# Kernel tuning notes

Hardware: AMD Instinct MI355X
Metric: run time of the kernel (lower is better)

Reference implementation:

```python
import jax, jax.numpy as jnp
import numpy as np

B, C, H, W = 16, 512, 25, 25
HEADS = 8
HID = 2048
PATCH = 5  # hardcoded patch_size in FusionAttention
EPS_LN = 1e-5
EPS_BN = 1e-5


def _channel_layernorm(x, g, b):
    # torch: std = var(unbiased=False).sqrt(); (x-mean)/(std+eps)*g + b, over channel dim=1
    mean = jnp.mean(x, axis=1, keepdims=True)
    var = jnp.var(x, axis=1, keepdims=True)
    return (x - mean) / (jnp.sqrt(var) + EPS_LN) * g + b


def _dwconv3x3(x, w, b):
    # depthwise 3x3, padding 1; w: (C,1,3,3)
    y = jax.lax.conv_general_dilated(
        x, w, window_strides=(1, 1), padding=((1, 1), (1, 1)),
        feature_group_count=x.shape[1],
        dimension_numbers=('NCHW', 'OIHW', 'NCHW'))
    return y + b[None, :, None, None]


def setup_inputs() -> dict:
    key = jax.random.key(0)
    ks = jax.random.split(key, 20)
    s = 0.02
    d = {
        'x': jax.random.normal(ks[0], (B, C, H, W), jnp.float32),
        'ln1_g': jnp.ones((1, C, 1, 1), jnp.float32),
        'ln1_b': jnp.zeros((1, C, 1, 1), jnp.float32),
        'wq': jax.random.normal(ks[1], (C, 1, 3, 3), jnp.float32) * s,
        'bq': jnp.zeros((C,), jnp.float32),
        'wk': jax.random.normal(ks[2], (C, 1, 3, 3), jnp.float32) * s,
        'bk': jnp.zeros((C,), jnp.float32),
        'wv': jax.random.normal(ks[3], (C, 1, 3, 3), jnp.float32) * s,
        'bv': jnp.zeros((C,), jnp.float32),
        'swq': jax.random.normal(ks[4], (C, 1, 3, 3), jnp.float32) * s,
        'sbq': jnp.zeros((C,), jnp.float32),
        'swk': jax.random.normal(ks[5], (C, 1, 3, 3), jnp.float32) * s,
        'sbk': jnp.zeros((C,), jnp.float32),
        'swv': jax.random.normal(ks[6], (C, 1, 3, 3), jnp.float32) * s,
        'sbv': jnp.zeros((C,), jnp.float32),
        'proj_w': jax.random.normal(ks[7], (C, C, 1, 1), jnp.float32) * s,
        'bn_g': jnp.ones((C,), jnp.float32),
        'bn_b': jnp.zeros((C,), jnp.float32),
        'bn_mean': jnp.zeros((C,), jnp.float32),
        'bn_var': jnp.ones((C,), jnp.float32),
        'ln2_g': jnp.ones((1, C, 1, 1), jnp.float32),
        'ln2_b': jnp.zeros((1, C, 1, 1), jnp.float32),
        'w1': jax.random.normal(ks[8], (HID, C, 1, 1), jnp.float32) * s,
        'b1': jnp.zeros((HID,), jnp.float32),
        'w2': jax.random.normal(ks[9], (C, HID, 1, 1), jnp.float32) * s,
        'b2': jnp.zeros((C,), jnp.float32),
    }
    return d


def _fusion_attention(x, wq, bq, wk, bk, wv, bv, swq, sbq, swk, sbk, swv, sbv,
                      proj_w, bn_g, bn_b, bn_mean, bn_var):
    b, c, h, w = x.shape
    n = h * w
    hd = c // HEADS
    scale = hd ** -0.5

    def split_heads(t):  # (b,c,h,w) -> (b, heads, n, hd)
        return t.reshape(b, HEADS, hd, n).transpose(0, 1, 3, 2)

    q = split_heads(_dwconv3x3(x, wq, bq))
    k = split_heads(_dwconv3x3(x, wk, bk))
    v = split_heads(_dwconv3x3(x, wv, bv))

    dots = jnp.einsum('bhid,bhjd->bhij', q, k) * scale
    attn = jax.nn.softmax(dots, axis=-1)
    out = jnp.einsum('bhij,bhjd->bhid', attn, v)
    # rearrange 'b h (H W) d -> b (h d) H W' with H=PATCH
    out = out.transpose(0, 1, 3, 2).reshape(b, c, PATCH, n // PATCH)

    spe_q = _dwconv3x3(out, swq, sbq).reshape(b, c, n)          # b d (l w)
    spe_k = _dwconv3x3(out, swk, sbk).reshape(b, c, n).transpose(0, 2, 1)  # b (l w) d
    spe_v = _dwconv3x3(out, swv, sbv).reshape(b, c, n)

    attention = jax.nn.softmax(jnp.einsum('bcn,bnd->bcd', spe_q, spe_k) * scale, axis=-1)
    x_out = jnp.einsum('bcd,bdn->bcn', attention, spe_v).reshape(b, c, h, w)

    # 1x1 conv (no bias) + BatchNorm2d (eval mode)
    proj = jnp.einsum('oc,bchw->bohw', proj_w[:, :, 0, 0], x_out)
    proj = (proj - bn_mean[None, :, None, None]) / jnp.sqrt(bn_var + EPS_BN)[None, :, None, None]
    proj = proj * bn_g[None, :, None, None] + bn_b[None, :, None, None]
    return proj


def _feedforward(x, w1, b1, w2, b2):
    h1 = jnp.einsum('oc,bchw->bohw', w1[:, :, 0, 0], x) + b1[None, :, None, None]
    h1 = jax.nn.gelu(h1, approximate=False)
    return jnp.einsum('oc,bchw->bohw', w2[:, :, 0, 0], h1) + b2[None, :, None, None]


def reference(x, ln1_g, ln1_b, wq, bq, wk, bk, wv, bv, swq, sbq, swk, sbk,
              swv, sbv, proj_w, bn_g, bn_b, bn_mean, bn_var, ln2_g, ln2_b,
              w1, b1, w2, b2):
    y1 = x + _fusion_attention(_channel_layernorm(x, ln1_g, ln1_b),
                               wq, bq, wk, bk, wv, bv, swq, sbq, swk, sbk,
                               swv, sbv, proj_w, bn_g, bn_b, bn_mean, bn_var)
    y_out = y1 + _feedforward(_channel_layernorm(y1, ln2_g, ln2_b), w1, b1, w2, b2)
    return y_out
```

## Files before the change

### kernel.cpp

```cpp
#include <hip/hip_runtime.h>
#include <math.h>

constexpr int BATCH = 16;
constexpr int CH    = 512;
constexpr int NPIX  = 625;
constexpr int HEADS = 8;
constexpr int HDIM  = 64;
constexpr int HIDD  = 2048;

constexpr float EPS_LN = 1e-5f;
constexpr float EPS_BN = 1e-5f;
constexpr float SCALE  = 0.125f;

typedef __bf16 bf16x8 __attribute__((ext_vector_type(8)));
typedef float  f32x4  __attribute__((ext_vector_type(4)));

static __device__ inline unsigned pack_bf16(float lo, float hi) {
  union { __bf16 h; unsigned short u; } a, b;
  a.h = (__bf16)lo; b.h = (__bf16)hi;
  return ((unsigned)b.u << 16) | (unsigned)a.u;
}

__global__ __launch_bounds__(256) void ln_kernel2(
    const float* __restrict__ x, const float* __restrict__ g,
    const float* __restrict__ bt, float* __restrict__ y) {
  __shared__ float ps[4][64];
  __shared__ float pss[4][64];
  int lane = threadIdx.x & 63;
  int w    = threadIdx.x >> 6;
  int b    = blockIdx.y;
  int i    = blockIdx.x * 64 + lane;
  int ic   = i < NPIX ? i : NPIX - 1;
  const float* xb = x + (size_t)b * CH * NPIX + ic;
  float s = 0.f, ss = 0.f;
  #pragma unroll 4
  for (int c = w * 128; c < w * 128 + 128; ++c) {
    float v = xb[(size_t)c * NPIX];
    s += v; ss += v * v;
  }
  ps[w][lane] = s; pss[w][lane] = ss;
  __syncthreads();
  float st  = ps[0][lane] + ps[1][lane] + ps[2][lane] + ps[3][lane];
  float sst = pss[0][lane] + pss[1][lane] + pss[2][lane] + pss[3][lane];
  float mean = st * (1.0f / CH);
  float var  = sst * (1.0f / CH) - mean * mean;
  float inv  = 1.0f / (sqrtf(fmaxf(var, 0.0f)) + EPS_LN);
  if (i >= NPIX) return;
  float* yb = y + (size_t)b * CH * NPIX + i;
  #pragma unroll 4
  for (int c = w * 128; c < w * 128 + 128; ++c) {
    float v = xb[(size_t)c * NPIX];
    yb[(size_t)c * NPIX] = (v - mean) * inv * g[c] + bt[c];
  }
}

__global__ void dwconv3_kernel(const float* __restrict__ src,
    const float* __restrict__ w0, const float* __restrict__ b0,
    const float* __restrict__ w1, const float* __restrict__ b1,
    const float* __restrict__ w2, const float* __restrict__ b2,
    float* __restrict__ d0, float* __restrict__ d1, float* __restrict__ d2,
    int Hc, int Wc) {
  size_t idx = (size_t)blockIdx.x * blockDim.x + threadIdx.x;
  size_t total = (size_t)BATCH * CH * Hc * Wc;
  if (idx >= total) return;
  int wp = (int)(idx % Wc);
  int hp = (int)((idx / Wc) % Hc);
  int c  = (int)((idx / ((size_t)Wc * Hc)) % CH);
  const float* f0 = w0 + c * 9;
  const float* f1 = w1 + c * 9;
  const float* f2 = w2 + c * 9;
  float a0 = 0.f, a1 = 0.f, a2 = 0.f;
  #pragma unroll
  for (int kh = -1; kh <= 1; ++kh) {
    int h2 = hp + kh; if (h2 < 0 || h2 >= Hc) continue;
    #pragma unroll
    for (int kw = -1; kw <= 1; ++kw) {
      int w2p = wp + kw; if (w2p < 0 || w2p >= Wc) continue;
      float v = src[idx + (size_t)kh * Wc + kw];
      int wi = (kh + 1) * 3 + (kw + 1);
      a0 += v * f0[wi]; a1 += v * f1[wi]; a2 += v * f2[wi];
    }
  }
  d0[idx] = a0 + b0[c];
  d1[idx] = a1 + b1[c];
  d2[idx] = a2 + b2[c];
}

__global__ void dwconv_spe_kernel(const float* __restrict__ src,
    const float* __restrict__ w0, const float* __restrict__ b0,
    const float* __restrict__ w1, const float* __restrict__ b1,
    const float* __restrict__ w2, const float* __restrict__ b2,
    __bf16* __restrict__ q16, __bf16* __restrict__ k16, float* __restrict__ v) {
  size_t idx = (size_t)blockIdx.x * blockDim.x + threadIdx.x;
  if (idx >= (size_t)BATCH * CH * 640) return;
  int n = (int)(idx % 640);
  int c = (int)((idx / 640) % CH);
  int b = (int)(idx / ((size_t)640 * CH));
  if (n >= NPIX) { q16[idx] = (__bf16)0.f; k16[idx] = (__bf16)0.f; return; }
  int hp = n / 125, wp = n % 125;
  size_t base = ((size_t)b * CH + c) * NPIX;
  const float* f0 = w0 + c * 9;
  const float* f1 = w1 + c * 9;
  const float* f2 = w2 + c * 9;
  float a0 = 0.f, a1 = 0.f, a2 = 0.f;
  #pragma unroll
  for (int kh = -1; kh <= 1; ++kh) {
    int h2 = hp + kh; if (h2 < 0 || h2 >= 5) continue;
    #pragma unroll
    for (int kw = -1; kw <= 1; ++kw) {
      int w2p = wp + kw; if (w2p < 0 || w2p >= 125) continue;
      float vv = src[base + h2 * 125 + w2p];
      int wi = (kh + 1) * 3 + (kw + 1);
      a0 += vv * f0[wi]; a1 += vv * f1[wi]; a2 += vv * f2[wi];
    }
  }
  q16[idx] = (__bf16)(a0 + b0[c]);
  k16[idx] = (__bf16)(a1 + b1[c]);
  v[base + n] = a2 + b2[c];
}

__global__ __launch_bounds__(256) void qk_to_bf16T(
    const float* __restrict__ q, const float* __restrict__ k,
    __bf16* __restrict__ qT, __bf16* __restrict__ kT) {
  __shared__ __bf16 tq[64][65];
  __shared__ __bf16 tk[64][65];
  int bh = blockIdx.y;
  int n0 = blockIdx.x * 64;
  int b = bh >> 3, h = bh & 7;
  const float* qb = q + (size_t)(b * CH + h * HDIM) * NPIX;
  const float* kb = k + (size_t)(b * CH + h * HDIM) * NPIX;
  #pragma unroll
  for (int it = 0; it < 16; ++it) {
    int idx = threadIdx.x + it * 256;
    int d = idx >> 6, n = idx & 63;
    int nn = n0 + n;
    float qv = (nn < NPIX) ? qb[(size_t)d * NPIX + nn] : 0.f;
    float kv = (nn < NPIX) ? kb[(size_t)d * NPIX + nn] : 0.f;
    tq[n][d] = (__bf16)qv;
    tk[n][d] = (__bf16)kv;
  }
  __syncthreads();
  size_t obase = (size_t)bh * NPIX;
  #pragma unroll
  for (int it = 0; it < 16; ++it) {
    int idx = threadIdx.x + it * 256;
    int n = idx >> 6, d = idx & 63;
    int nn = n0 + n;
    if (nn < NPIX) {
      qT[(obase + nn) * 64 + d] = tq[n][d];
      kT[(obase + nn) * 64 + d] = tk[n][d];
    }
  }
}

__global__ void v_to_bf16(const float* __restrict__ v, __bf16* __restrict__ v16) {
  int row = blockIdx.x;
  const float* src = v + (size_t)row * NPIX;
  __bf16* dst = v16 + (size_t)row * 640;
  for (int n = threadIdx.x; n < NPIX; n += 256) dst[n] = (__bf16)src[n];
}

__global__ __launch_bounds__(64) void head_attn_mfma2(
    const __bf16* __restrict__ qT, const __bf16* __restrict__ kT,
    const __bf16* __restrict__ vB, float* __restrict__ out) {
  __shared__ __align__(16) union SmT {
    unsigned char p[16 * 1280];
    float ostage[64][17];
  } sm;
  int lane = threadIdx.x & 63;
  int g = lane >> 4, li = lane & 15;
  int h = blockIdx.y, b = blockIdx.z;
  int bh = b * HEADS + h;
  int i0 = blockIdx.x * 16;
  const __bf16* Qb = qT + (size_t)bh * NPIX * 64;
  const __bf16* Kb = kT + (size_t)bh * NPIX * 64;
  const __bf16* Vb = vB + (size_t)(b * CH + h * HDIM) * 640;

  bf16x8 aq0, aq1;
  {
    int qr = i0 + li; if (qr > NPIX - 1) qr = NPIX - 1;
    const __bf16* qp = Qb + (size_t)qr * 64 + 8 * g;
    aq0 = *(const bf16x8*)(qp);
    aq1 = *(const bf16x8*)(qp + 32);
  }

  f32x4 s[40];
  #pragma unroll
  for (int cf = 0; cf < 40; ++cf) {
    int kc = cf * 16 + li;
    int kcl = kc > NPIX - 1 ? NPIX - 1 : kc;
    const __bf16* kp = Kb + (size_t)kcl * 64 + 8 * g;
    bf16x8 bk0 = *(const bf16x8*)(kp);
    bf16x8 bk1 = *(const bf16x8*)(kp + 32);
    f32x4 acc = (f32x4){0.f, 0.f, 0.f, 0.f};
    acc = __builtin_amdgcn_mfma_f32_16x16x32_bf16(aq0, bk0, acc, 0, 0, 0);
    acc = __builtin_amdgcn_mfma_f32_16x16x32_bf16(aq1, bk1, acc, 0, 0, 0);
    s[cf] = acc * SCALE;
  }
  if (li > 0) {
    s[39][0] = -1e30f; s[39][1] = -1e30f; s[39][2] = -1e30f; s[39][3] = -1e30f;
  }

  #pragma unroll
  for (int r = 0; r < 4; ++r) {
    float mx = -1e30f;
    #pragma unroll
    for (int cf = 0; cf < 40; ++cf) mx = fmaxf(mx, s[cf][r]);
    mx = fmaxf(mx, __shfl_xor(mx, 1));
    mx = fmaxf(mx, __shfl_xor(mx, 2));
    mx = fmaxf(mx, __shfl_xor(mx, 4));
    mx = fmaxf(mx, __shfl_xor(mx, 8));
    float sum = 0.f;
    #pragma unroll
    for (int cf = 0; cf < 40; ++cf) {
      float p = __expf(s[cf][r] - mx);
      s[cf][r] = p;
      sum += p;
    }
    sum += __shfl_xor(sum, 1);
    sum += __shfl_xor(sum, 2);
    sum += __shfl_xor(sum, 4);
    sum += __shfl_xor(sum, 8);
    float inv = 1.0f / sum;
    #pragma unroll
    for (int cf = 0; cf < 40; ++cf) s[cf][r] *= inv;
  }

  #pragma unroll
  for (int cfp = 0; cfp < 20; ++cfp) {
    int cf0 = 2 * cfp, cf1 = cf0 + 1;
    #pragma unroll
    for (int r = 0; r < 4; ++r) {
      float v0 = s[cf0][r], v1 = s[cf1][r];
      float t0 = __shfl_xor(v0, 1);
      float t1 = __shfl_xor(v1, 1);
      bool even = (li & 1) == 0;
      float lo = even ? v0 : t1;
      float hi = even ? t0 : v1;
      int col_w = even ? (cf0 * 16 + li) : (cf1 * 16 + li - 1);
      int row = 4 * g + r;
      int off = (row * 1280 + col_w * 2) ^ ((row & 7) << 4);
      *(unsigned*)(&sm.p[off]) = pack_bf16(lo, hi);
    }
  }

  f32x4 o[4];
  #pragma unroll
  for (int dg = 0; dg < 4; ++dg) o[dg] = (f32x4){0.f, 0.f, 0.f, 0.f};
  #pragma unroll
  for (int ks = 0; ks < 20; ++ks) {
    int offr = (li * 1280 + ks * 64 + 16 * g) ^ ((li & 7) << 4);
    bf16x8 pa = *(const bf16x8*)(&sm.p[offr]);
    const __bf16* vp = Vb + (size_t)li * 640 + ks * 32 + 8 * g;
    #pragma unroll
    for (int dg = 0; dg < 4; ++dg) {
      bf16x8 bv = *(const bf16x8*)(vp + (size_t)dg * 16 * 640);
      o[dg] = __builtin_amdgcn_mfma_f32_16x16x32_bf16(pa, bv, o[dg], 0, 0, 0);
    }
  }

  __syncthreads();
  #pragma unroll
  for (int dg = 0; dg < 4; ++dg) {
    #pragma unroll
    for (int r = 0; r < 4; ++r)
      sm.ostage[dg * 16 + li][4 * g + r] = o[dg][r];
  }
  __syncthreads();
  size_t cbase = (size_t)(b * CH + h * HDIM);
  int n = i0 + li;
  if (n < NPIX) {
    #pragma unroll
    for (int dd = 0; dd < 16; ++dd) {
      int d = dd * 4 + g;
      out[(cbase + d) * NPIX + n] = sm.ostage[d][li];
    }
  }
}

__global__ __launch_bounds__(64) void chan_attn_mfma(
    const __bf16* __restrict__ sq, const __bf16* __restrict__ sk,
    __bf16* __restrict__ Am) {
  int lane = threadIdx.x & 63;
  int g = lane >> 4, li = lane & 15;
  int b = blockIdx.y;
  int cq0 = blockIdx.x * 16;
  const __bf16* qrow  = sq + ((size_t)b * CH + cq0 + li) * 640 + 8 * g;
  const __bf16* kbase = sk + ((size_t)b * CH + li) * 640 + 8 * g;
  f32x4 acc[32];
  #pragma unroll
  for (int i = 0; i < 32; ++i) acc[i] = (f32x4){0.f, 0.f, 0.f, 0.f};
  for (int ks = 0; ks < 20; ++ks) {
    bf16x8 af = *(const bf16x8*)(qrow + ks * 32);
    #pragma unroll
    for (int cf = 0; cf < 32; ++cf) {
      bf16x8 bfr = *(const bf16x8*)(kbase + (size_t)cf * 16 * 640 + ks * 32);
      acc[cf] = __builtin_amdgcn_mfma_f32_16x16x32_bf16(af, bfr, acc[cf], 0, 0, 0);
    }
  }
  #pragma unroll
  for (int i = 0; i < 32; ++i) acc[i] = acc[i] * SCALE;
  __bf16* Ab = Am + ((size_t)b * CH + cq0) * CH;
  #pragma unroll
  for (int r = 0; r < 4; ++r) {
    float mx = -1e30f;
    #pragma unroll
    for (int cf = 0; cf < 32; ++cf) mx = fmaxf(mx, acc[cf][r]);
    mx = fmaxf(mx, __shfl_xor(mx, 1));
    mx = fmaxf(mx, __shfl_xor(mx, 2));
    mx = fmaxf(mx, __shfl_xor(mx, 4));
    mx = fmaxf(mx, __shfl_xor(mx, 8));
    float sum = 0.f;
    #pragma unroll
    for (int cf = 0; cf < 32; ++cf) {
      float p = __expf(acc[cf][r] - mx);
      acc[cf][r] = p;
      sum += p;
    }
    sum += __shfl_xor(sum, 1);
    sum += __shfl_xor(sum, 2);
    sum += __shfl_xor(sum, 4);
    sum += __shfl_xor(sum, 8);
    float inv = 1.0f / sum;
    #pragma unroll
    for (int cf = 0; cf < 32; ++cf)
      Ab[(size_t)(4 * g + r) * CH + cf * 16 + li] = (__bf16)(acc[cf][r] * inv);
  }
}

template <int EPI>
__global__ __launch_bounds__(256) void gemm_nt(
    const __bf16* __restrict__ A, long long aBatch,
    const __bf16* __restrict__ B, long long bBatch,
    void* __restrict__ Cout, long long cBatch,
    int M, int N, int K,
    const float* __restrict__ p0, const float* __restrict__ p1,
    const float* __restrict__ res, long long resBatch) {
  __shared__ __align__(16) union {
    struct { unsigned char As[128 * 128]; unsigned char Bs[64 * 128]; } s;
    float Ce[4][64][17];
  } u;
  int t = threadIdx.x;
  int w = t >> 6, lane = t & 63, g = lane >> 4, li = lane & 15;
  int wm = w & 1, wn = w >> 1;
  int n0 = blockIdx.x * 64, m0 = blockIdx.y * 128, b = blockIdx.z;
  const __bf16* Ab = A + (size_t)b * aBatch;
  const __bf16* Bb = B + (size_t)b * bBatch;
  f32x4 acc[4][2];
  #pragma unroll
  for (int i = 0; i < 4; ++i)
    #pragma unroll
    for (int j = 0; j < 2; ++j) acc[i][j] = (f32x4){0.f, 0.f, 0.f, 0.f};

  for (int k0 = 0; k0 < K; k0 += 64) {
    bf16x8 ra[4], rb[2];
    #pragma unroll
    for (int i = 0; i < 4; ++i) {
      int e = t + i * 256;
      int row = e >> 3, cc = e & 7;
      int ar = m0 + row; ar = ar < M ? ar : M - 1;
      ra[i] = *(const bf16x8*)(Ab + (size_t)ar * K + k0 + cc * 8);
    }
    #pragma unroll
    for (int i = 0; i < 2; ++i) {
      int e = t + i * 256;
      int row = e >> 3, cc = e & 7;
      rb[i] = *(const bf16x8*)(Bb + (size_t)(n0 + row) * K + k0 + cc * 8);
    }
    __syncthreads();
    #pragma unroll
    for (int i = 0; i < 4; ++i) {
      int e = t + i * 256; int row = e >> 3, cc = e & 7;
      int off = (row * 128 + cc * 16) ^ ((row & 7) << 4);
      *(bf16x8*)(&u.s.As[off]) = ra[i];
    }
    #pragma unroll
    for (int i = 0; i < 2; ++i) {
      int e = t + i * 256; int row = e >> 3, cc = e & 7;
      int off = (row * 128 + cc * 16) ^ ((row & 7) << 4);
      *(bf16x8*)(&u.s.Bs[off]) = rb[i];
    }
    __syncthreads();
    #pragma unroll
    for (int ks = 0; ks < 2; ++ks) {
      bf16x8 af[4], bfr[2];
      #pragma unroll
      for (int mf = 0; mf < 4; ++mf) {
        int row = wm * 64 + mf * 16 + li;
        int off = (row * 128 + ks * 64 + g * 16) ^ ((row & 7) << 4);
        af[mf] = *(const bf16x8*)(&u.s.As[off]);
      }
      #pragma unroll
      for (int nf = 0; nf < 2; ++nf) {
        int row = wn * 32 + nf * 16 + li;
        int off = (row * 128 + ks * 64 + g * 16) ^ ((row & 7) << 4);
        bfr[nf] = *(const bf16x8*)(&u.s.Bs[off]);
      }
      #pragma unroll
      for (int mf = 0; mf < 4; ++mf)
        #pragma unroll
        for (int nf = 0; nf < 2; ++nf)
          acc[mf][nf] = __builtin_amdgcn_mfma_f32_16x16x32_bf16(
              af[mf], bfr[nf], acc[mf][nf], 0, 0, 0);
    }
    __syncthreads();
  }

  #pragma unroll
  for (int p = 0; p < 2; ++p) {
    __syncthreads();
    #pragma unroll
    for (int mf = 0; mf < 4; ++mf) {
      #pragma unroll
      for (int r = 0; r < 4; ++r)
        u.Ce[w][mf * 16 + 4 * g + r][li] = acc[mf][p][r];
    }
    __syncthreads();
    int m = m0 + wm * 64 + lane;
    int colb = n0 + wn * 32 + p * 16;
    if (m < M) {
      float vv[16];
      #pragma unroll
      for (int c = 0; c < 16; ++c) vv[c] = u.Ce[w][lane][c];
      if (EPI == 0) {
        __bf16* Cb = (__bf16*)Cout + (size_t)b * cBatch + (size_t)m * N + colb;
        bf16x8 o0, o1;
        #pragma unroll
        for (int j = 0; j < 8; ++j) { o0[j] = (__bf16)vv[j]; o1[j] = (__bf16)vv[8 + j]; }
        *(bf16x8*)(Cb) = o0;
        *(bf16x8*)(Cb + 8) = o1;
      } else if (EPI == 1) {
        float* Cf = (float*)Cout + (size_t)b * cBatch + (size_t)m * N + colb;
        const float* rp = res + (size_t)b * resBatch + (size_t)m * N + colb;
        #pragma unroll
        for (int c = 0; c < 16; ++c)
          vv[c] = vv[c] * p0[colb + c] + p1[colb + c] + rp[c];
        #pragma unroll
        for (int c4 = 0; c4 < 4; ++c4)
          *(f32x4*)(Cf + c4 * 4) = (f32x4){vv[c4*4], vv[c4*4+1], vv[c4*4+2], vv[c4*4+3]};
      } else if (EPI == 2) {
        __bf16* Cb = (__bf16*)Cout + (size_t)b * cBatch + (size_t)m * N + colb;
        #pragma unroll
        for (int c = 0; c < 16; ++c) {
          float xg = vv[c] + p0[colb + c];
          vv[c] = 0.5f * xg * (1.0f + erff(xg * 0.70710678118654752f));
        }
        bf16x8 o0, o1;
        #pragma unroll
        for (int j = 0; j < 8; ++j) { o0[j] = (__bf16)vv[j]; o1[j] = (__bf16)vv[8 + j]; }
        *(bf16x8*)(Cb) = o0;
        *(bf16x8*)(Cb + 8) = o1;
      } else {
        float* Cf = (float*)Cout + (size_t)b * cBatch + (size_t)m * N + colb;
        const float* rp = res + (size_t)b * resBatch + (size_t)m * N + colb;
        #pragma unroll
        for (int c = 0; c < 16; ++c)
          vv[c] = vv[c] + p0[colb + c] + rp[c];
        #pragma unroll
        for (int c4 = 0; c4 < 4; ++c4)
          *(f32x4*)(Cf + c4 * 4) = (f32x4){vv[c4*4], vv[c4*4+1], vv[c4*4+2], vv[c4*4+3]};
      }
    }
  }
}

template <typename TO>
__global__ __launch_bounds__(256) void transpose_bat(
    const float* __restrict__ in, TO* __restrict__ out, int R, int Cc) {
  __shared__ float tile[64][65];
  int b = blockIdx.z;
  int c0 = blockIdx.x * 64, r0 = blockIdx.y * 64;
  const float* ib = in + (size_t)b * R * Cc;
  TO* ob = out + (size_t)b * R * Cc;
  for (int e = threadIdx.x; e < 4096; e += 256) {
    int rr = e >> 6, cc = e & 63;
    int r = r0 + rr, c = c0 + cc;
    tile[rr][cc] = (r < R && c < Cc) ? ib[(size_t)r * Cc + c] : 0.f;
  }
  __syncthreads();
  for (int e = threadIdx.x; e < 4096; e += 256) {
    int cc = e >> 6, rr = e & 63;
    int r = r0 + rr, c = c0 + cc;
    if (r < R && c < Cc) ob[(size_t)c * R + r] = (TO)tile[rr][cc];
  }
}

__global__ __launch_bounds__(256) void ln2_row_kernel(
    const float* __restrict__ y, const float* __restrict__ g,
    const float* __restrict__ bt, __bf16* __restrict__ o) {
  int row = blockIdx.x * 4 + (threadIdx.x >> 6);
  int lane = threadIdx.x & 63;
  const float* yr = y + (size_t)row * CH + lane * 8;
  f32x4 v0 = *(const f32x4*)(yr);
  f32x4 v1 = *(const f32x4*)(yr + 4);
  float s = v0[0]+v0[1]+v0[2]+v0[3]+v1[0]+v1[1]+v1[2]+v1[3];
  float ss = v0[0]*v0[0]+v0[1]*v0[1]+v0[2]*v0[2]+v0[3]*v0[3]
           + v1[0]*v1[0]+v1[1]*v1[1]+v1[2]*v1[2]+v1[3]*v1[3];
  #pragma unroll
  for (int off = 32; off > 0; off >>= 1) {
    s  += __shfl_xor(s, off);
    ss += __shfl_xor(ss, off);
  }
  float mean = s * (1.0f / CH);
  float var  = ss * (1.0f / CH) - mean * mean;
  float inv  = 1.0f / (sqrtf(fmaxf(var, 0.0f)) + EPS_LN);
  f32x4 g0 = *(const f32x4*)(g + lane * 8);
  f32x4 g1 = *(const f32x4*)(g + lane * 8 + 4);
  f32x4 b0 = *(const f32x4*)(bt + lane * 8);
  f32x4 b1 = *(const f32x4*)(bt + lane * 8 + 4);
  bf16x8 ov;
  #pragma unroll
  for (int j = 0; j < 4; ++j) ov[j]     = (__bf16)((v0[j] - mean) * inv * g0[j] + b0[j]);
  #pragma unroll
  for (int j = 0; j < 4; ++j) ov[4 + j] = (__bf16)((v1[j] - mean) * inv * g1[j] + b1[j]);
  *(bf16x8*)(o + (size_t)row * CH + lane * 8) = ov;
}

__global__ void cast_bf16_kernel(const float* __restrict__ s, __bf16* __restrict__ d, int n) {
  int i = blockIdx.x * 256 + threadIdx.x;
  if (i < n) d[i] = (__bf16)s[i];
}

__global__ void bn_prep(const float* __restrict__ g, const float* __restrict__ bt,
                        const float* __restrict__ mean, const float* __restrict__ var,
                        float* __restrict__ scale, float* __restrict__ shift) {
  int c = blockIdx.x * blockDim.x + threadIdx.x;
  if (c >= CH) return;
  float s = g[c] * rsqrtf(var[c] + EPS_BN);
  scale[c] = s;
  shift[c] = bt[c] - mean[c] * s;
}

extern "C" void kernel_launch(void* const* d_in, const int* in_sizes, int n_in,
                              void* d_out, int out_size, void* d_ws, size_t ws_size,
                              hipStream_t stream) {
  const float* x      = (const float*)d_in[0];
  const float* ln1_g  = (const float*)d_in[1];
  const float* ln1_b  = (const float*)d_in[2];
  const float* wq     = (const float*)d_in[3];
  const float* bq     = (const float*)d_in[4];
  const float* wk     = (const float*)d_in[5];
  const float* bk     = (const float*)d_in[6];
  const float* wv     = (const float*)d_in[7];
  const float* bv     = (const float*)d_in[8];
  const float* swq    = (const float*)d_in[9];
  const float* sbq    = (const float*)d_in[10];
  const float* swk    = (const float*)d_in[11];
  const float* sbk    = (const float*)d_in[12];
  const float* swv    = (const float*)d_in[13];
  const float* sbv    = (const float*)d_in[14];
  const float* proj_w = (const float*)d_in[15];
  const float* bn_g   = (const float*)d_in[16];
  const float* bn_b   = (const float*)d_in[17];
  const float* bn_m   = (const float*)d_in[18];
  const float* bn_v   = (const float*)d_in[19];
  const float* ln2_g  = (const float*)d_in[20];
  const float* ln2_b  = (const float*)d_in[21];
  const float* w1     = (const float*)d_in[22];
  const float* b1     = (const float*)d_in[23];
  const float* w2     = (const float*)d_in[24];
  const float* b2     = (const float*)d_in[25];

  char* W = (char*)d_ws;
  const size_t SZB = 20480000;
  char* S0 = W;
  char* S1 = W + SZB;
  char* S2 = W + 2 * SZB;
  char* S3 = W + 3 * SZB;
  char* S4 = W + 4 * SZB;

  float*  xln   = (float*)S0;
  float*  qb    = (float*)S1;
  float*  kb    = (float*)S2;
  float*  vb    = (float*)S3;
  __bf16* qT    = (__bf16*)S0;
  __bf16* kTp   = qT + (size_t)BATCH * HEADS * NPIX * 64;
  __bf16* v16   = (__bf16*)d_out;
  float*  ab    = (float*)S4;
  __bf16* sq16  = (__bf16*)S1;
  __bf16* sk16  = (__bf16*)S2;
  float*  sv    = (float*)S3;
  __bf16* svT   = (__bf16*)S4;
  __bf16* Amat  = (__bf16*)S0;
  __bf16* pw16  = (__bf16*)(S0 + 10485760);
  __bf16* w116  = (__bf16*)(S0 + 10485760 + 524288);
  __bf16* w216  = (__bf16*)(S0 + 10485760 + 524288 + 2097152);
  float*  bnsc  = (float*)(S0 + 10485760 + 524288 + 2097152 + 2097152);
  float*  bnsh  = bnsc + CH;
  __bf16* xoutT = (__bf16*)S1;
  float*  x_nc  = (float*)S4;
  float*  y1_nc = (float*)S3;
  __bf16* y1ln  = (__bf16*)S0;
  __bf16* h1T   = (__bf16*)S1;
  float*  tmp_nc = (float*)S4;

  const size_t SZ = (size_t)BATCH * CH * NPIX;

  ln_kernel2<<<dim3(10, BATCH), 256, 0, stream>>>(x, ln1_g, ln1_b, xln);
  dwconv3_kernel<<<(int)((SZ + 255) / 256), 256, 0, stream>>>(
      xln, wq, bq, wk, bk, wv, bv, qb, kb, vb, 25, 25);
  qk_to_bf16T<<<dim3(10, BATCH * HEADS), 256, 0, stream>>>(qb, kb, qT, kTp);
  v_to_bf16<<<dim3(BATCH * CH), 256, 0, stream>>>(vb, v16);
  head_attn_mfma2<<<dim3(40, HEADS, BATCH), 64, 0, stream>>>(qT, kTp, v16, ab);
  dwconv_spe_kernel<<<(int)(((size_t)BATCH * CH * 640 + 255) / 256), 256, 0, stream>>>(
      ab, swq, sbq, swk, sbk, swv, sbv, sq16, sk16, sv);
  transpose_bat<__bf16><<<dim3(10, 8, BATCH), 256, 0, stream>>>(sv, svT, CH, NPIX);
  cast_bf16_kernel<<<1024, 256, 0, stream>>>(proj_w, pw16, CH * CH);
  cast_bf16_kernel<<<4096, 256, 0, stream>>>(w1, w116, HIDD * CH);
  cast_bf16_kernel<<<4096, 256, 0, stream>>>(w2, w216, CH * HIDD);
  bn_prep<<<2, 256, 0, stream>>>(bn_g, bn_b, bn_m, bn_v, bnsc, bnsh);
  chan_attn_mfma<<<dim3(32, BATCH), 64, 0, stream>>>(sq16, sk16, Amat);
  gemm_nt<0><<<dim3(8, 5, BATCH), 256, 0, stream>>>(
      svT, (long long)NPIX * CH, Amat, (long long)CH * CH,
      xoutT, (long long)NPIX * CH, NPIX, CH, CH,
      nullptr, nullptr, nullptr, 0);
  transpose_bat<float><<<dim3(10, 8, BATCH), 256, 0, stream>>>(x, x_nc, CH, NPIX);
  gemm_nt<1><<<dim3(8, 79, 1), 256, 0, stream>>>(
      xoutT, 0LL, pw16, 0LL, y1_nc, 0LL, BATCH * NPIX, CH, CH,
      bnsc, bnsh, x_nc, 0LL);
  ln2_row_kernel<<<BATCH * NPIX / 4, 256, 0, stream>>>(y1_nc, ln2_g, ln2_b, y1ln);
  gemm_nt<2><<<dim3(32, 79, 1), 256, 0, stream>>>(
      y1ln, 0LL, w116, 0LL, h1T, 0LL, BATCH * NPIX, HIDD, CH,
      b1, nullptr, nullptr, 0LL);
  gemm_nt<3><<<dim3(8, 79, 1), 256, 0, stream>>>(
      h1T, 0LL, w216, 0LL, tmp_nc, 0LL, BATCH * NPIX, CH, HIDD,
      b2, nullptr, y1_nc, 0LL);
  transpose_bat<float><<<dim3(8, 10, BATCH), 256, 0, stream>>>(
      tmp_nc, (float*)d_out, NPIX, CH);
}
```

Measured before the change: 600.7 us.

## Split head attention across four waves per block with shared softmax reduction

The per-head spatial attention kernel now runs four waves per block instead of one. Each wave computes a quarter of the key columns for the QK scores, and the row max and sum are combined through shared memory. The P·V product is split so each wave produces 16 of the 64 output channels. This cuts per-thread register pressure (10 score fragments instead of 40) and raises parallelism, at the cost of extra __syncthreads and scalar bf16 shared stores in place of the swizzled packed writes.

```diff
diff --git a/kernel.cpp b/kernel.cpp
--- a/kernel.cpp
+++ b/kernel.cpp
@@ -14,12 +14,6 @@
 
 typedef __bf16 bf16x8 __attribute__((ext_vector_type(8)));
 typedef float  f32x4  __attribute__((ext_vector_type(4)));
-
-static __device__ inline unsigned pack_bf16(float lo, float hi) {
-  union { __bf16 h; unsigned short u; } a, b;
-  a.h = (__bf16)lo; b.h = (__bf16)hi;
-  return ((unsigned)b.u << 16) | (unsigned)a.u;
-}
 
 __global__ __launch_bounds__(256) void ln_kernel2(
     const float* __restrict__ x, const float* __restrict__ g,
@@ -160,21 +154,23 @@
   for (int n = threadIdx.x; n < NPIX; n += 256) dst[n] = (__bf16)src[n];
 }
 
-__global__ __launch_bounds__(64) void head_attn_mfma2(
+__global__ __launch_bounds__(256) void head_attn_mfma3(
     const __bf16* __restrict__ qT, const __bf16* __restrict__ kT,
     const __bf16* __restrict__ vB, float* __restrict__ out) {
-  __shared__ __align__(16) union SmT {
-    unsigned char p[16 * 1280];
+  __shared__ __align__(16) union SmU {
+    unsigned char p[16 * 1296];
     float ostage[64][17];
   } sm;
-  int lane = threadIdx.x & 63;
-  int g = lane >> 4, li = lane & 15;
+  __shared__ float red_max[4][16];
+  __shared__ float red_sum[4][16];
+
+  int t = threadIdx.x;
+  int w = t >> 6, lane = t & 63, g = lane >> 4, li = lane & 15;
   int h = blockIdx.y, b = blockIdx.z;
   int bh = b * HEADS + h;
   int i0 = blockIdx.x * 16;
   const __bf16* Qb = qT + (size_t)bh * NPIX * 64;
   const __bf16* Kb = kT + (size_t)bh * NPIX * 64;
-  const __bf16* Vb = vB + (size_t)(b * CH + h * HDIM) * 640;
 
   bf16x8 aq0, aq1;
   {
@@ -184,97 +180,90 @@
     aq1 = *(const bf16x8*)(qp + 32);
   }
 
-  f32x4 s[40];
-  #pragma unroll
-  for (int cf = 0; cf < 40; ++cf) {
-    int kc = cf * 16 + li;
+  f32x4 s[10];
+  #pragma unroll
+  for (int cfl = 0; cfl < 10; ++cfl) {
+    int kc = (w * 10 + cfl) * 16 + li;
     int kcl = kc > NPIX - 1 ? NPIX - 1 : kc;
     const __bf16* kp = Kb + (size_t)kcl * 64 + 8 * g;
     bf16x8 bk0 = *(const bf16x8*)(kp);
     bf16x8 bk1 = *(const bf16x8*)(kp + 32);
-    f32x4 acc = (f32x4){0.f, 0.f, 0.f, 0.f};
-    acc = __builtin_amdgcn_mfma_f32_16x16x32_bf16(aq0, bk0, acc, 0, 0, 0);
-    acc = __builtin_amdgcn_mfma_f32_16x16x32_bf16(aq1, bk1, acc, 0, 0, 0);
-    s[cf] = acc * SCALE;
-  }
-  if (li > 0) {
-    s[39][0] = -1e30f; s[39][1] = -1e30f; s[39][2] = -1e30f; s[39][3] = -1e30f;
+    f32x4 a = (f32x4){0.f, 0.f, 0.f, 0.f};
+    a = __builtin_amdgcn_mfma_f32_16x16x32_bf16(aq0, bk0, a, 0, 0, 0);
+    a = __builtin_amdgcn_mfma_f32_16x16x32_bf16(aq1, bk1, a, 0, 0, 0);
+    s[cfl] = a * SCALE;
+  }
+  if (w == 3 && li > 0) {
+    s[9][0] = -1e30f; s[9][1] = -1e30f; s[9][2] = -1e30f; s[9][3] = -1e30f;
   }
 
   #pragma unroll
   for (int r = 0; r < 4; ++r) {
-    float mx = -1e30f;
-    #pragma unroll
-    for (int cf = 0; cf < 40; ++cf) mx = fmaxf(mx, s[cf][r]);
+    float mx = s[0][r];
+    #pragma unroll
+    for (int cfl = 1; cfl < 10; ++cfl) mx = fmaxf(mx, s[cfl][r]);
     mx = fmaxf(mx, __shfl_xor(mx, 1));
     mx = fmaxf(mx, __shfl_xor(mx, 2));
     mx = fmaxf(mx, __shfl_xor(mx, 4));
     mx = fmaxf(mx, __shfl_xor(mx, 8));
+    if (li == 0) red_max[w][4 * g + r] = mx;
+  }
+  __syncthreads();
+
+  #pragma unroll
+  for (int r = 0; r < 4; ++r) {
+    int row = 4 * g + r;
+    float mx = fmaxf(fmaxf(red_max[0][row], red_max[1][row]),
+                     fmaxf(red_max[2][row], red_max[3][row]));
     float sum = 0.f;
     #pragma unroll
-    for (int cf = 0; cf < 40; ++cf) {
-      float p = __expf(s[cf][r] - mx);
-      s[cf][r] = p;
+    for (int cfl = 0; cfl < 10; ++cfl) {
+      float p = __expf(s[cfl][r] - mx);
+      s[cfl][r] = p;
       sum += p;
     }
     sum += __shfl_xor(sum, 1);
     sum += __shfl_xor(sum, 2);
     sum += __shfl_xor(sum, 4);
     sum += __shfl_xor(sum, 8);
-    float inv = 1.0f / sum;
-    #pragma unroll
-    for (int cf = 0; cf < 40; ++cf) s[cf][r] *= inv;
-  }
-
-  #pragma unroll
-  for (int cfp = 0; cfp < 20; ++cfp) {
-    int cf0 = 2 * cfp, cf1 = cf0 + 1;
-    #pragma unroll
-    for (int r = 0; r < 4; ++r) {
-      float v0 = s[cf0][r], v1 = s[cf1][r];
-      float t0 = __shfl_xor(v0, 1);
-      float t1 = __shfl_xor(v1, 1);
-      bool even = (li & 1) == 0;
-      float lo = even ? v0 : t1;
-      float hi = even ? t0 : v1;
-      int col_w = even ? (cf0 * 16 + li) : (cf1 * 16 + li - 1);
-      int row = 4 * g + r;
-      int off = (row * 1280 + col_w * 2) ^ ((row & 7) << 4);
-      *(unsigned*)(&sm.p[off]) = pack_bf16(lo, hi);
-    }
-  }
-
-  f32x4 o[4];
-  #pragma unroll
-  for (int dg = 0; dg < 4; ++dg) o[dg] = (f32x4){0.f, 0.f, 0.f, 0.f};
+    if (li == 0) red_sum[w][row] = sum;
+  }
+  __syncthreads();
+
+  #pragma unroll
+  for (int r = 0; r < 4; ++r) {
+    int row = 4 * g + r;
+    float l = red_sum[0][row] + red_sum[1][row] + red_sum[2][row] + red_sum[3][row];
+    float inv = 1.0f / l;
+    #pragma unroll
+    for (int cfl = 0; cfl < 10; ++cfl) {
+      int col = (w * 10 + cfl) * 16 + li;
+      *(__bf16*)(&sm.p[row * 1296 + col * 2]) = (__bf16)(s[cfl][r] * inv);
+    }
+  }
+  __syncthreads();
+
+  const __bf16* vrow = vB + (size_t)(b * CH + h * HDIM + w * 16 + li) * 640;
+  f32x4 o = (f32x4){0.f, 0.f, 0.f, 0.f};
   #pragma unroll
   for (int ks = 0; ks < 20; ++ks) {
-    int offr = (li * 1280 + ks * 64 + 16 * g) ^ ((li & 7) << 4);
-    bf16x8 pa = *(const bf16x8*)(&sm.p[offr]);
-    const __bf16* vp = Vb + (size_t)li * 640 + ks * 32 + 8 * g;
-    #pragma unroll
-    for (int dg = 0; dg < 4; ++dg) {
-      bf16x8 bv = *(const bf16x8*)(vp + (size_t)dg * 16 * 640);
-      o[dg] = __builtin_amdgcn_mfma_f32_16x16x32_bf16(pa, bv, o[dg], 0, 0, 0);
-    }
-  }
-
-  __syncthreads();
-  #pragma unroll
-  for (int dg = 0; dg < 4; ++dg) {
-    #pragma unroll
-    for (int r = 0; r < 4; ++r)
-      sm.ostage[dg * 16 + li][4 * g + r] = o[dg][r];
-  }
+    bf16x8 pa = *(const bf16x8*)(&sm.p[li * 1296 + ks * 64 + 16 * g]);
+    bf16x8 bv = *(const bf16x8*)(vrow + ks * 32 + 8 * g);
+    o = __builtin_amdgcn_mfma_f32_16x16x32_bf16(pa, bv, o, 0, 0, 0);
+  }
+  __syncthreads();
+
+  #pragma unroll
+  for (int r = 0; r < 4; ++r)
+    sm.ostage[w * 16 + li][4 * g + r] = o[r];
   __syncthreads();
   size_t cbase = (size_t)(b * CH + h * HDIM);
-  int n = i0 + li;
-  if (n < NPIX) {
-    #pragma unroll
-    for (int dd = 0; dd < 16; ++dd) {
-      int d = dd * 4 + g;
-      out[(cbase + d) * NPIX + n] = sm.ostage[d][li];
-    }
+  #pragma unroll
+  for (int it = 0; it < 4; ++it) {
+    int e = t + it * 256;
+    int d = e >> 4, nl = e & 15;
+    int n = i0 + nl;
+    if (n < NPIX) out[(cbase + d) * NPIX + n] = sm.ostage[d][nl];
   }
 }
 
@@ -601,7 +590,7 @@
       xln, wq, bq, wk, bk, wv, bv, qb, kb, vb, 25, 25);
   qk_to_bf16T<<<dim3(10, BATCH * HEADS), 256, 0, stream>>>(qb, kb, qT, kTp);
   v_to_bf16<<<dim3(BATCH * CH), 256, 0, stream>>>(vb, v16);
-  head_attn_mfma2<<<dim3(40, HEADS, BATCH), 64, 0, stream>>>(qT, kTp, v16, ab);
+  head_attn_mfma3<<<dim3(40, HEADS, BATCH), 256, 0, stream>>>(qT, kTp, v16, ab);
   dwconv_spe_kernel<<<(int)(((size_t)BATCH * CH * 640 + 255) / 256), 256, 0, stream>>>(
       ab, swq, sbq, swk, sbk, swv, sbv, sq16, sk16, sv);
   transpose_bat<__bf16><<<dim3(10, 8, BATCH), 256, 0, stream>>>(sv, svT, CH, NPIX);
```

Measured after the change: 592.6 us. Within noise of the previous version (-1.4%).
